# Optimization experiments

Measured on AMD Instinct MI355X. Metric: run time of the kernel, lower is better.

Reference implementation:

```python
import jax, jax.numpy as jnp
import numpy as np

N = 50000
F = 128
E = 800000
HOP = 3
ALPHA = 0.2  # leaky relu slope


def setup_inputs() -> dict:
    key = jax.random.key(0)
    ks = jax.random.split(key, 6)
    x = jax.random.normal(ks[0], (N, F), dtype=jnp.float32)
    h0 = jax.random.normal(ks[1], (N, F), dtype=jnp.float32)
    edge_index = jax.random.randint(ks[2], (2, E), 0, N, dtype=jnp.int32)
    edge_weight = jax.random.uniform(ks[3], (E,), dtype=jnp.float32)
    # xavier-uniform-ish params
    lim_w = float(np.sqrt(6.0 / (F + F)))
    W_att = jax.random.uniform(ks[4], (F, F), dtype=jnp.float32, minval=-lim_w, maxval=lim_w)
    lim_a = 1.414 * float(np.sqrt(6.0 / (2 * F + 1)))
    a = jax.random.uniform(ks[5], (2 * F, 1), dtype=jnp.float32, minval=-lim_a, maxval=lim_a)
    temp = jnp.zeros((4,), dtype=jnp.float32)
    return {"x": x, "h0": h0, "edge_index": edge_index, "edge_weight": edge_weight,
            "W_att": W_att, "a": a, "temp": temp}


def _segment_softmax(e, rows, num_segments):
    m = jax.ops.segment_max(e, rows, num_segments=num_segments)
    m = jnp.where(jnp.isfinite(m), m, 0.0)  # guard empty rows
    ex = jnp.exp(e - m[rows])
    s = jax.ops.segment_sum(ex, rows, num_segments=num_segments)
    s = jnp.where(s > 0, s, 1.0)
    return ex / s[rows]


def reference(x, h0, edge_index, edge_weight, W_att, a, temp):
    rows, cols = edge_index[0], edge_index[1]
    # --- attention (edge-wise, never materializing dense NxN e) ---
    feat = x @ W_att                       # [N, F]
    f1 = (feat @ a[:F]).squeeze(-1)        # [N]
    f2 = (feat @ a[F:]).squeeze(-1)        # [N]
    e = f1[rows] + f2[cols]                # e[i,j] at edges
    e = jnp.where(e > 0, e, ALPHA * e)     # leaky relu
    att = _segment_softmax(e, rows, N)     # sparse row softmax values
    P = 0.5 * att
    # --- lifting bases ---
    coe = jax.nn.sigmoid(temp)
    rowsum = jax.ops.segment_sum(edge_weight * P, rows, num_segments=N)  # [N]
    update = x
    feat_prime = None
    for step in range(HOP):
        # sparse mm: U @ update
        update = jax.ops.segment_sum(att[:, None] * update[cols], rows, num_segments=N)
        feat_even = coe[0] * x + update
        feat_odd = update - feat_even * rowsum[:, None]
        feat_prime = feat_odd if step == 0 else coe[2] * feat_prime + (1.0 - coe[2]) * feat_odd
    return feat_prime
```

## Files before the change

kernel.cpp:

```cpp
#include <hip/hip_runtime.h>
#include <hip/hip_fp16.h>

#define NN 50000
#define FF 128
#define EE 800000
#define ALPHA 0.2f
#define ESHIFT 4.0f

#define NBINS 196
#define CAPB 5120
#define EPB 2048
#define BCAP 6144

union H2 { unsigned u; int i; __half2 h; };
union G4 { uint4 u; __half2 h2[4]; };

__global__ void k_w(const float* __restrict__ W, const float* __restrict__ a,
                    float* __restrict__ w12, int* __restrict__ bin_fill) {
    int k = threadIdx.x;
    for (int i = k; i < NBINS; i += 128) bin_fill[i] = 0;
    float s1 = 0.f, s2 = 0.f;
    const float* wr = W + k * FF;
    for (int j = 0; j < FF; ++j) {
        float w = wr[j];
        s1 += w * a[j];
        s2 += w * a[FF + j];
    }
    w12[k] = s1;
    w12[FF + k] = s2;
}

__global__ void k_f(const float* __restrict__ x, const float* __restrict__ w12,
                    float* __restrict__ f1, float* __restrict__ f2,
                    __half* __restrict__ xh) {
    int gid = blockIdx.x * blockDim.x + threadIdx.x;
    int node = gid >> 6;
    int lane = threadIdx.x & 63;
    if (node >= NN) return;
    float2 xv = ((const float2*)(x + (size_t)node * FF))[lane];
    ((__half2*)(xh + (size_t)node * FF))[lane] = __float22half2_rn(xv);
    float2 w1 = ((const float2*)w12)[lane];
    float2 w2 = ((const float2*)(w12 + FF))[lane];
    float s1 = xv.x * w1.x + xv.y * w1.y;
    float s2 = xv.x * w2.x + xv.y * w2.y;
#pragma unroll
    for (int o = 32; o > 0; o >>= 1) {
        s1 += __shfl_down(s1, o);
        s2 += __shfl_down(s2, o);
    }
    if (lane == 0) { f1[node] = s1; f2[node] = s2; }
}

__global__ void k_bin(const int* __restrict__ rows, const int* __restrict__ cols,
                      const float* __restrict__ ew, const float* __restrict__ f1,
                      const float* __restrict__ f2, int* __restrict__ bin_fill,
                      int2* __restrict__ binbuf) {
    __shared__ int cnt[NBINS];
    __shared__ int gbase[NBINS];
    int tid = threadIdx.x;
    if (tid < NBINS) cnt[tid] = 0;
    __syncthreads();
    int e0 = blockIdx.x * EPB;
    int rk[8], bn[8], rc[8], pay[8];
    bool vl[8];
#pragma unroll
    for (int k = 0; k < 8; ++k) {
        int e = e0 + k * 256 + tid;
        vl[k] = e < EE;
        if (vl[k]) {
            int r = rows[e], c = cols[e];
            float v = f1[r] + f2[c];
            v = v > 0.f ? v : ALPHA * v;
            float ex = __expf(v - ESHIFT);
            H2 p;
            p.h = __floats2half2_rn(ex, ew[e] * ex);
            pay[k] = p.i;
            rc[k] = (r << 16) | c;
            bn[k] = r >> 8;
            rk[k] = atomicAdd(&cnt[bn[k]], 1);
        }
    }
    __syncthreads();
    if (tid < NBINS) {
        int c0 = cnt[tid];
        gbase[tid] = c0 ? atomicAdd(&bin_fill[tid], c0) : 0;
    }
    __syncthreads();
#pragma unroll
    for (int k = 0; k < 8; ++k) {
        if (vl[k]) {
            int pos = gbase[bn[k]] + rk[k];
            if (pos < CAPB) binbuf[(size_t)bn[k] * CAPB + pos] = make_int2(rc[k], pay[k]);
        }
    }
}

__global__ void k_csr(const int* __restrict__ bin_fill, const int2* __restrict__ binbuf,
                      int2* __restrict__ csr, unsigned* __restrict__ csr2,
                      int2* __restrict__ rowinfo, float* __restrict__ rs) {
    __shared__ int lfill[256];
    __shared__ int pbeg[256];
    __shared__ int cursor[256];
    __shared__ int wsum[4];
    int tid = threadIdx.x;
    int lane = tid & 63, wave = tid >> 6;
    int bin = blockIdx.x;
    int cnt = bin_fill[bin];
    if (cnt > CAPB) cnt = CAPB;
    lfill[tid] = 0;
    __syncthreads();
    const int2* bb = binbuf + (size_t)bin * CAPB;
    for (int i = tid; i < cnt; i += 256) {
        atomicAdd(&lfill[(bb[i].x >> 16) & 0xFF], 1);
    }
    __syncthreads();
    int pc = (lfill[tid] + 3) & ~3;
    int s = pc;
#pragma unroll
    for (int o = 1; o < 64; o <<= 1) {
        int t = __shfl_up(s, o);
        if (lane >= o) s += t;
    }
    if (lane == 63) wsum[wave] = s;
    __syncthreads();
    int woff = 0;
#pragma unroll
    for (int i = 0; i < 4; ++i)
        if (i < wave) woff += wsum[i];
    int binbase = bin * BCAP;
    int beg = binbase + woff + (s - pc);
    pbeg[tid] = beg;
    cursor[tid] = beg;
    __syncthreads();
    for (int i = tid; i < cnt; i += 256) {
        int2 e = bb[i];
        int rl = (e.x >> 16) & 0xFF;
        int p = atomicAdd(&cursor[rl], 1);
        csr[p] = make_int2(e.x & 0xFFFF, e.y);
    }
    __syncthreads();
    int r = (bin << 8) + tid;
    if (r < NN) {
        int b0 = pbeg[tid];
        int dreal = lfill[tid];
        int dpad = (dreal + 3) & ~3;
        float se = 0.f, sw = 0.f;
        for (int i = 0; i < dreal; ++i) {
            H2 pu;
            pu.i = csr[b0 + i].y;
            float2 f = __half22float2(pu.h);
            se += f.x;
            sw += f.y;
        }
        float inv = se > 0.f ? 1.f / se : 0.f;
        rs[r] = 0.5f * sw * inv;
        for (int i = 0; i < dreal; ++i) {
            int2 e = csr[b0 + i];
            H2 pu;
            pu.i = e.y;
            float att = __half22float2(pu.h).x * inv;
            unsigned ab = (unsigned)__half_as_ushort(__float2half_rn(att));
            csr2[b0 + i] = (unsigned)e.x | (ab << 16);
        }
        for (int i = dreal; i < dpad; ++i) csr2[b0 + i] = 0u;
        rowinfo[r] = make_int2(b0, dpad);
    }
}

__device__ __forceinline__ void emit_row(
    int step, int r, int fl, const float* ax, float se,
    __half* __restrict__ uout, __half* __restrict__ S, const float* __restrict__ rs,
    const float* __restrict__ x, float* __restrict__ out,
    float w0, float w1c, float w2c, float coe0)
{
    float inv = se > 0.f ? 1.f / se : 0.f;
    float a[8];
#pragma unroll
    for (int k = 0; k < 8; ++k) a[k] = ax[k] * inv;
    if (step == 0) {
        G4 o1, o2;
#pragma unroll
        for (int t = 0; t < 4; ++t) {
            o1.h2[t] = __floats2half2_rn(a[2 * t], a[2 * t + 1]);
            o2.h2[t] = __floats2half2_rn(w0 * a[2 * t], w0 * a[2 * t + 1]);
        }
        ((uint4*)(uout + (size_t)r * FF))[fl] = o1.u;
        ((uint4*)(S + (size_t)r * FF))[fl] = o2.u;
    } else if (step == 1) {
        G4 o1, sv;
        sv.u = ((const uint4*)(S + (size_t)r * FF))[fl];
#pragma unroll
        for (int t = 0; t < 4; ++t) {
            o1.h2[t] = __floats2half2_rn(a[2 * t], a[2 * t + 1]);
            float2 svf = __half22float2(sv.h2[t]);
            sv.h2[t] = __floats2half2_rn(svf.x + w1c * a[2 * t],
                                         svf.y + w1c * a[2 * t + 1]);
        }
        ((uint4*)(uout + (size_t)r * FF))[fl] = o1.u;
        ((uint4*)(S + (size_t)r * FF))[fl] = sv.u;
    } else {
        float rsv = rs[r];
        float k1 = 1.f - rsv, k2 = coe0 * rsv;
        G4 sv;
        sv.u = ((const uint4*)(S + (size_t)r * FF))[fl];
        const float4* xr = (const float4*)(x + (size_t)r * FF);
        float4* orow = (float4*)(out + (size_t)r * FF);
        float4 xv0 = xr[2 * fl], xv1 = xr[2 * fl + 1];
        float res[8];
#pragma unroll
        for (int t = 0; t < 4; ++t) {
            float2 svf = __half22float2(sv.h2[t]);
            res[2 * t] = k1 * (svf.x + w2c * a[2 * t]);
            res[2 * t + 1] = k1 * (svf.y + w2c * a[2 * t + 1]);
        }
        orow[2 * fl] = make_float4(res[0] - k2 * xv0.x, res[1] - k2 * xv0.y,
                                   res[2] - k2 * xv0.z, res[3] - k2 * xv0.w);
        orow[2 * fl + 1] = make_float4(res[4] - k2 * xv1.x, res[5] - k2 * xv1.y,
                                       res[6] - k2 * xv1.z, res[7] - k2 * xv1.w);
    }
}

__global__ __launch_bounds__(256) void k_hop(
    const float* __restrict__ x, const __half* __restrict__ uin,
    __half* __restrict__ uout, const int2* __restrict__ rowinfo,
    const unsigned* __restrict__ csr2, const float* __restrict__ temp,
    const float* __restrict__ rs, __half* __restrict__ S,
    float* __restrict__ out, int step)
{
    int wave = threadIdx.x >> 6;
    int lane = threadIdx.x & 63;
    int r = blockIdx.x * 4 + wave;
    if (r >= NN) return;
    int s = lane >> 4;
    int fl = lane & 15;
    int2 ri = rowinfo[r];
    const unsigned* bk = csr2 + ri.x;
    int d = ri.y;
    float ax[8];
#pragma unroll
    for (int k = 0; k < 8; ++k) ax[k] = 0.f;
    float se = 0.f;
    for (int j = 0; j < d; j += 16) {
        unsigned b[4];
        G4 g[4];
#pragma unroll
        for (int gi = 0; gi < 4; ++gi) {
            int e = j + 4 * gi + s;
            b[gi] = e < d ? bk[e] : 0u;
        }
#pragma unroll
        for (int gi = 0; gi < 4; ++gi)
            g[gi].u = ((const uint4*)(uin + (size_t)(b[gi] & 0xFFFF) * FF))[fl];
#pragma unroll
        for (int gi = 0; gi < 4; ++gi) {
            H2 p;
            p.u = b[gi] >> 16;
            float at = __half22float2(p.h).x;
            se += at;
#pragma unroll
            for (int t = 0; t < 4; ++t) {
                float2 uv = __half22float2(g[gi].h2[t]);
                ax[2 * t] += at * uv.x;
                ax[2 * t + 1] += at * uv.y;
            }
        }
    }
#pragma unroll
    for (int o = 16; o < 64; o <<= 1) {
#pragma unroll
        for (int k = 0; k < 8; ++k) ax[k] += __shfl_xor(ax[k], o);
        se += __shfl_xor(se, o);
    }
    if (s == 0) {
        float c2 = 1.f / (1.f + __expf(-temp[2]));
        float coe0 = 1.f / (1.f + __expf(-temp[0]));
        float w0 = c2 * c2, w1c = c2 * (1.f - c2), w2c = 1.f - c2;
        emit_row(step, r, fl, ax, se, uout, S, rs, x, out, w0, w1c, w2c, coe0);
    }
}

extern "C" void kernel_launch(void* const* d_in, const int* in_sizes, int n_in,
                              void* d_out, int out_size, void* d_ws, size_t ws_size,
                              hipStream_t stream) {
    const float* x = (const float*)d_in[0];
    const int* eidx = (const int*)d_in[2];
    const int* rows = eidx;
    const int* cols = eidx + EE;
    const float* ew = (const float*)d_in[3];
    const float* W = (const float*)d_in[4];
    const float* a = (const float*)d_in[5];
    const float* temp = (const float*)d_in[6];
    float* out = (float*)d_out;

    float* ws = (float*)d_ws;
    int* bin_fill = (int*)ws;
    float* w12 = ws + 256;
    float* f1 = ws + 512;
    float* f2 = f1 + NN;
    float* rs = f2 + NN;
    int2* rowinfo = (int2*)(rs + NN);
    int2* csr = rowinfo + NN;
    unsigned* csr2 = (unsigned*)(csr + (size_t)NBINS * BCAP);
    __half* xh = (__half*)(csr2 + (size_t)NBINS * BCAP);
    __half* uh0 = xh + (size_t)NN * FF;
    __half* Sb = uh0 + (size_t)NN * FF;
    int2* binbuf = (int2*)Sb;
    __half* uh1 = xh;

    k_w<<<1, 128, 0, stream>>>(W, a, w12, bin_fill);
    k_f<<<(NN + 3) / 4, 256, 0, stream>>>(x, w12, f1, f2, xh);
    k_bin<<<(EE + EPB - 1) / EPB, 256, 0, stream>>>(rows, cols, ew, f1, f2, bin_fill, binbuf);
    k_csr<<<NBINS, 256, 0, stream>>>(bin_fill, binbuf, csr, csr2, rowinfo, rs);
    k_hop<<<(NN + 3) / 4, 256, 0, stream>>>(x, xh, uh0, rowinfo, csr2, temp, rs, Sb, out, 0);
    k_hop<<<(NN + 3) / 4, 256, 0, stream>>>(x, uh0, uh1, rowinfo, csr2, temp, rs, Sb, out, 1);
    k_hop<<<(NN + 3) / 4, 256, 0, stream>>>(x, uh1, uh0, rowinfo, csr2, temp, rs, Sb, out, 2);
}
```

Measured before the change: 263.4 us.

## Replace binned CSR build with fixed-capacity per-row buckets via global atomics

Drops the two-pass bin-then-sort CSR construction and has each edge claim a slot in a fixed 64-entry per-row bucket with a global atomic on a degree counter. A new per-row normalisation kernel then reduces the softmax denominator and weighted row sum with wave shuffles and writes the packed column/attention entries. The hop kernels index rows at a fixed stride instead of reading a row-info table. This trades the shared-memory binning and sorting passes for many scattered global atomics and a larger padded layout, and silently drops edges beyond 64 per row.

```diff
diff --git a/kernel.cpp b/kernel.cpp
--- a/kernel.cpp
+++ b/kernel.cpp
@@ -6,19 +6,15 @@
 #define EE 800000
 #define ALPHA 0.2f
 #define ESHIFT 4.0f
-
-#define NBINS 196
-#define CAPB 5120
-#define EPB 2048
-#define BCAP 6144
+#define RCAP 64
 
 union H2 { unsigned u; int i; __half2 h; };
 union G4 { uint4 u; __half2 h2[4]; };
+union HF { float f; int i; };
 
 __global__ void k_w(const float* __restrict__ W, const float* __restrict__ a,
-                    float* __restrict__ w12, int* __restrict__ bin_fill) {
+                    float* __restrict__ w12) {
     int k = threadIdx.x;
-    for (int i = k; i < NBINS; i += 128) bin_fill[i] = 0;
     float s1 = 0.f, s2 = 0.f;
     const float* wr = W + k * FF;
     for (int j = 0; j < FF; ++j) {
@@ -32,10 +28,14 @@
 
 __global__ void k_f(const float* __restrict__ x, const float* __restrict__ w12,
                     float* __restrict__ f1, float* __restrict__ f2,
-                    __half* __restrict__ xh) {
+                    __half* __restrict__ xh, int* __restrict__ deg) {
     int gid = blockIdx.x * blockDim.x + threadIdx.x;
     int node = gid >> 6;
     int lane = threadIdx.x & 63;
+    if (threadIdx.x < 4) {
+        int dr = blockIdx.x * 4 + threadIdx.x;
+        if (dr < NN) deg[dr] = 0;
+    }
     if (node >= NN) return;
     float2 xv = ((const float2*)(x + (size_t)node * FF))[lane];
     ((__half2*)(xh + (size_t)node * FF))[lane] = __float22half2_rn(xv);
@@ -51,120 +51,66 @@
     if (lane == 0) { f1[node] = s1; f2[node] = s2; }
 }
 
-__global__ void k_bin(const int* __restrict__ rows, const int* __restrict__ cols,
-                      const float* __restrict__ ew, const float* __restrict__ f1,
-                      const float* __restrict__ f2, int* __restrict__ bin_fill,
-                      int2* __restrict__ binbuf) {
-    __shared__ int cnt[NBINS];
-    __shared__ int gbase[NBINS];
-    int tid = threadIdx.x;
-    if (tid < NBINS) cnt[tid] = 0;
-    __syncthreads();
-    int e0 = blockIdx.x * EPB;
-    int rk[8], bn[8], rc[8], pay[8];
-    bool vl[8];
-#pragma unroll
-    for (int k = 0; k < 8; ++k) {
-        int e = e0 + k * 256 + tid;
-        vl[k] = e < EE;
-        if (vl[k]) {
-            int r = rows[e], c = cols[e];
-            float v = f1[r] + f2[c];
-            v = v > 0.f ? v : ALPHA * v;
-            float ex = __expf(v - ESHIFT);
-            H2 p;
-            p.h = __floats2half2_rn(ex, ew[e] * ex);
-            pay[k] = p.i;
-            rc[k] = (r << 16) | c;
-            bn[k] = r >> 8;
-            rk[k] = atomicAdd(&cnt[bn[k]], 1);
-        }
-    }
-    __syncthreads();
-    if (tid < NBINS) {
-        int c0 = cnt[tid];
-        gbase[tid] = c0 ? atomicAdd(&bin_fill[tid], c0) : 0;
-    }
-    __syncthreads();
-#pragma unroll
-    for (int k = 0; k < 8; ++k) {
-        if (vl[k]) {
-            int pos = gbase[bn[k]] + rk[k];
-            if (pos < CAPB) binbuf[(size_t)bn[k] * CAPB + pos] = make_int2(rc[k], pay[k]);
-        }
-    }
-}
-
-__global__ void k_csr(const int* __restrict__ bin_fill, const int2* __restrict__ binbuf,
-                      int2* __restrict__ csr, unsigned* __restrict__ csr2,
-                      int2* __restrict__ rowinfo, float* __restrict__ rs) {
-    __shared__ int lfill[256];
-    __shared__ int pbeg[256];
-    __shared__ int cursor[256];
-    __shared__ int wsum[4];
-    int tid = threadIdx.x;
-    int lane = tid & 63, wave = tid >> 6;
-    int bin = blockIdx.x;
-    int cnt = bin_fill[bin];
-    if (cnt > CAPB) cnt = CAPB;
-    lfill[tid] = 0;
-    __syncthreads();
-    const int2* bb = binbuf + (size_t)bin * CAPB;
-    for (int i = tid; i < cnt; i += 256) {
-        atomicAdd(&lfill[(bb[i].x >> 16) & 0xFF], 1);
-    }
-    __syncthreads();
-    int pc = (lfill[tid] + 3) & ~3;
-    int s = pc;
+__global__ __launch_bounds__(256) void k_bin2(
+    const int* __restrict__ rows, const int* __restrict__ cols,
+    const float* __restrict__ ew, const float* __restrict__ f1,
+    const float* __restrict__ f2, int* __restrict__ deg, int2* __restrict__ ubuf)
+{
+    int e = blockIdx.x * 256 + threadIdx.x;
+    if (e >= EE) return;
+    int r = rows[e], c = cols[e];
+    float v = f1[r] + f2[c];
+    v = v > 0.f ? v : ALPHA * v;
+    float ex = __expf(v - ESHIFT);
+    unsigned exh = (unsigned)__half_as_ushort(__float2half_rn(ex));
+    int pos = atomicAdd(&deg[r], 1);
+    if (pos < RCAP) {
+        HF y;
+        y.f = ew[e] * ex;
+        ubuf[(size_t)r * RCAP + pos] = make_int2((int)((unsigned)c | (exh << 16)), y.i);
+    }
+}
+
+__global__ __launch_bounds__(256) void k_norm(
+    const int2* __restrict__ ubuf, const int* __restrict__ deg,
+    unsigned* __restrict__ csr2, float* __restrict__ rs, int* __restrict__ dpad)
+{
+    int wave = threadIdx.x >> 6, lane = threadIdx.x & 63;
+    int r = blockIdx.x * 4 + wave;
+    if (r >= NN) return;
+    int d = deg[r];
+    if (d > RCAP) d = RCAP;
+    int2 en = make_int2(0, 0);
+    if (lane < d) en = ubuf[(size_t)r * RCAP + lane];
+    float exf = 0.f, ewex = 0.f;
+    if (lane < d) {
+        H2 p;
+        p.u = ((unsigned)en.x) >> 16;
+        exf = __half22float2(p.h).x;
+        HF y;
+        y.i = en.y;
+        ewex = y.f;
+    }
 #pragma unroll
     for (int o = 1; o < 64; o <<= 1) {
-        int t = __shfl_up(s, o);
-        if (lane >= o) s += t;
-    }
-    if (lane == 63) wsum[wave] = s;
-    __syncthreads();
-    int woff = 0;
-#pragma unroll
-    for (int i = 0; i < 4; ++i)
-        if (i < wave) woff += wsum[i];
-    int binbase = bin * BCAP;
-    int beg = binbase + woff + (s - pc);
-    pbeg[tid] = beg;
-    cursor[tid] = beg;
-    __syncthreads();
-    for (int i = tid; i < cnt; i += 256) {
-        int2 e = bb[i];
-        int rl = (e.x >> 16) & 0xFF;
-        int p = atomicAdd(&cursor[rl], 1);
-        csr[p] = make_int2(e.x & 0xFFFF, e.y);
-    }
-    __syncthreads();
-    int r = (bin << 8) + tid;
-    if (r < NN) {
-        int b0 = pbeg[tid];
-        int dreal = lfill[tid];
-        int dpad = (dreal + 3) & ~3;
-        float se = 0.f, sw = 0.f;
-        for (int i = 0; i < dreal; ++i) {
-            H2 pu;
-            pu.i = csr[b0 + i].y;
-            float2 f = __half22float2(pu.h);
-            se += f.x;
-            sw += f.y;
-        }
-        float inv = se > 0.f ? 1.f / se : 0.f;
-        rs[r] = 0.5f * sw * inv;
-        for (int i = 0; i < dreal; ++i) {
-            int2 e = csr[b0 + i];
-            H2 pu;
-            pu.i = e.y;
-            float att = __half22float2(pu.h).x * inv;
-            unsigned ab = (unsigned)__half_as_ushort(__float2half_rn(att));
-            csr2[b0 + i] = (unsigned)e.x | (ab << 16);
-        }
-        for (int i = dreal; i < dpad; ++i) csr2[b0 + i] = 0u;
-        rowinfo[r] = make_int2(b0, dpad);
-    }
+        exf += __shfl_xor(exf, o);
+        ewex += __shfl_xor(ewex, o);
+    }
+    float inv = exf > 0.f ? 1.f / exf : 0.f;
+    int dp = (d + 3) & ~3;
+    if (lane == 0) {
+        rs[r] = 0.5f * ewex * inv;
+        dpad[r] = dp;
+    }
+    unsigned outv = 0u;
+    if (lane < d) {
+        H2 p;
+        p.u = ((unsigned)en.x) >> 16;
+        float att = __half22float2(p.h).x * inv;
+        outv = ((unsigned)en.x & 0xFFFFu) |
+               ((unsigned)__half_as_ushort(__float2half_rn(att)) << 16);
+    }
+    if (lane < dp) csr2[(size_t)r * RCAP + lane] = outv;
 }
 
 __device__ __forceinline__ void emit_row(
@@ -222,7 +168,7 @@
 
 __global__ __launch_bounds__(256) void k_hop(
     const float* __restrict__ x, const __half* __restrict__ uin,
-    __half* __restrict__ uout, const int2* __restrict__ rowinfo,
+    __half* __restrict__ uout, const int* __restrict__ dpad,
     const unsigned* __restrict__ csr2, const float* __restrict__ temp,
     const float* __restrict__ rs, __half* __restrict__ S,
     float* __restrict__ out, int step)
@@ -233,9 +179,8 @@
     if (r >= NN) return;
     int s = lane >> 4;
     int fl = lane & 15;
-    int2 ri = rowinfo[r];
-    const unsigned* bk = csr2 + ri.x;
-    int d = ri.y;
+    const unsigned* bk = csr2 + (size_t)r * RCAP;
+    int d = dpad[r];
     float ax[8];
 #pragma unroll
     for (int k = 0; k < 8; ++k) ax[k] = 0.f;
@@ -293,25 +238,24 @@
     float* out = (float*)d_out;
 
     float* ws = (float*)d_ws;
-    int* bin_fill = (int*)ws;
-    float* w12 = ws + 256;
-    float* f1 = ws + 512;
+    float* w12 = ws;
+    float* f1 = ws + 256;
     float* f2 = f1 + NN;
     float* rs = f2 + NN;
-    int2* rowinfo = (int2*)(rs + NN);
-    int2* csr = rowinfo + NN;
-    unsigned* csr2 = (unsigned*)(csr + (size_t)NBINS * BCAP);
-    __half* xh = (__half*)(csr2 + (size_t)NBINS * BCAP);
+    int* deg = (int*)(rs + NN);
+    int* dpad = deg + NN;
+    int2* ubuf = (int2*)(dpad + NN);
+    unsigned* csr2 = (unsigned*)(ubuf + (size_t)NN * RCAP);
+    __half* xh = (__half*)(csr2 + (size_t)NN * RCAP);
     __half* uh0 = xh + (size_t)NN * FF;
     __half* Sb = uh0 + (size_t)NN * FF;
-    int2* binbuf = (int2*)Sb;
     __half* uh1 = xh;
 
-    k_w<<<1, 128, 0, stream>>>(W, a, w12, bin_fill);
-    k_f<<<(NN + 3) / 4, 256, 0, stream>>>(x, w12, f1, f2, xh);
-    k_bin<<<(EE + EPB - 1) / EPB, 256, 0, stream>>>(rows, cols, ew, f1, f2, bin_fill, binbuf);
-    k_csr<<<NBINS, 256, 0, stream>>>(bin_fill, binbuf, csr, csr2, rowinfo, rs);
-    k_hop<<<(NN + 3) / 4, 256, 0, stream>>>(x, xh, uh0, rowinfo, csr2, temp, rs, Sb, out, 0);
-    k_hop<<<(NN + 3) / 4, 256, 0, stream>>>(x, uh0, uh1, rowinfo, csr2, temp, rs, Sb, out, 1);
-    k_hop<<<(NN + 3) / 4, 256, 0, stream>>>(x, uh1, uh0, rowinfo, csr2, temp, rs, Sb, out, 2);
-}
+    k_w<<<1, 128, 0, stream>>>(W, a, w12);
+    k_f<<<(NN + 3) / 4, 256, 0, stream>>>(x, w12, f1, f2, xh, deg);
+    k_bin2<<<(EE + 255) / 256, 256, 0, stream>>>(rows, cols, ew, f1, f2, deg, ubuf);
+    k_norm<<<(NN + 3) / 4, 256, 0, stream>>>(ubuf, deg, csr2, rs, dpad);
+    k_hop<<<(NN + 3) / 4, 256, 0, stream>>>(x, xh, uh0, dpad, csr2, temp, rs, Sb, out, 0);
+    k_hop<<<(NN + 3) / 4, 256, 0, stream>>>(x, uh0, uh1, dpad, csr2, temp, rs, Sb, out, 1);
+    k_hop<<<(NN + 3) / 4, 256, 0, stream>>>(x, uh1, uh0, dpad, csr2, temp, rs, Sb, out, 2);
+}
```

Measured after the change: 290.0 us. 1.1x slower.
